# Optimization experiments

Measured on AMD Instinct MI355X. Metric: run time of the kernel, lower is better.

Reference implementation:

```python
import jax, jax.numpy as jnp
import numpy as np

EPS = 1e-7  # K.epsilon()
ROUTINGS = 3


def squash(v, axis=-1):
    s2 = jnp.sum(jnp.square(v), axis=axis, keepdims=True)
    scale = s2 / (1.0 + s2) / jnp.sqrt(s2 + EPS)
    return scale * v


def setup_inputs() -> dict:
    key = jax.random.key(0)
    k1, k2 = jax.random.split(key)
    B, I, D, O, K = 64, 2048, 8, 32, 16
    x = jax.random.normal(k1, (B, I, D), dtype=jnp.float32)
    W = jax.random.normal(k2, (I, O, D, K), dtype=jnp.float32) * 0.05
    return {"x": x, "W": W}


def reference(x, W):
    # u_hat[b,o,i,k] = sum_d x[b,i,d] * W[i,o,d,k]
    u_hat = jnp.einsum('bid,iodk->boik', x, W)  # [B, O, I, K]
    B, O, I, _ = u_hat.shape
    b = jnp.zeros((B, O, I), dtype=u_hat.dtype)
    v = None
    for i in range(ROUTINGS):
        c = jax.nn.softmax(b, axis=1)                      # over output capsules
        s = jnp.einsum('boi,boik->bok', c, u_hat)          # weighted sum
        v = squash(s)                                      # [B, O, K]
        if i < ROUTINGS - 1:
            agreement = jnp.einsum('boik,bok->boi', u_hat, v)
            b = b + agreement
    return v
```

## Files before the change

### kernel.cpp

```cpp
#include <hip/hip_runtime.h>


__device__ __forceinline__ float4 f4add(float4 a, float4 b) {
    return make_float4(a.x + b.x, a.y + b.y, a.z + b.z, a.w + b.w);
}

template<int PASS0>
__global__ __launch_bounds__(512, 4)
void pass_kernel(const float* __restrict__ x,
                 const float* __restrict__ W,
                 const float* __restrict__ vin,
                 float* __restrict__ part)
{
    __shared__ __align__(16) float x_lds[32 * 64];
    __shared__ __align__(16) float red[8 * 2 * 512];
    __shared__ __align__(16) float vg[2 * 512];

    const int t  = threadIdx.x;
    const int w  = t >> 6;
    const int l  = t & 63;
    const int o  = l & 31;
    const int kk = l >> 5;
    const int bx = blockIdx.x;
    const int ch = bx & 255;
    const int h  = bx >> 8;
    const int i  = ch * 8 + w;

    float Wr[8][8];
    {
        const float* wp = W + (size_t)(i * 32 + o) * 128 + kk * 8;
        #pragma unroll
        for (int d = 0; d < 8; ++d) {
            float4 a = *(const float4*)(wp + d * 16);
            float4 b = *(const float4*)(wp + d * 16 + 4);
            Wr[d][0] = a.x; Wr[d][1] = a.y; Wr[d][2] = a.z; Wr[d][3] = a.w;
            Wr[d][4] = b.x; Wr[d][5] = b.y; Wr[d][6] = b.z; Wr[d][7] = b.w;
        }
        #pragma unroll
        for (int d = 0; d < 8; ++d)
            #pragma unroll
            for (int j = 0; j < 8; ++j)
                asm volatile("" : "+v"(Wr[d][j]));
    }
    {
        const int f  = t * 4;
        const int bl = f >> 6, r = f & 63;
        *(float4*)&x_lds[f] =
            *(const float4*)(x + (size_t)(h * 32 + bl) * 16384 + ch * 64 + r);
    }

    for (int g = 0; g < 16; ++g) {
        if (!PASS0) {
            if (t < 256) {
                const int bq = t >> 7, idx = t & 127;
                const int b  = h * 32 + g * 2 + bq;
                *(float4*)&vg[bq * 512 + idx * 4] =
                    *(const float4*)(vin + (size_t)b * 512 + idx * 4);
            }
        }
        __syncthreads();

        #pragma unroll
        for (int bq = 0; bq < 2; ++bq) {
            const int bl = g * 2 + bq;
            float4 xa = *(const float4*)&x_lds[bl * 64 + w * 8];
            float4 xb = *(const float4*)&x_lds[bl * 64 + w * 8 + 4];
            float xr[8] = {xa.x, xa.y, xa.z, xa.w, xb.x, xb.y, xb.z, xb.w};
            float uh[8];
            #pragma unroll
            for (int j = 0; j < 8; ++j) uh[j] = 0.f;
            #pragma unroll
            for (int d = 0; d < 8; ++d) {
                #pragma unroll
                for (int j = 0; j < 8; ++j)
                    uh[j] = fmaf(xr[d], Wr[d][j], uh[j]);
            }
            float c;
            if (PASS0) {
                c = 0.03125f;
            } else {
                float logit = 0.f;
                #pragma unroll
                for (int j = 0; j < 8; ++j)
                    logit = fmaf(uh[j], vg[bq * 512 + (kk * 8 + j) * 32 + o], logit);
                logit += __shfl_xor(logit, 32, 64);
                float ex = __expf(logit);
                float sm = ex;
                #pragma unroll
                for (int off = 16; off >= 1; off >>= 1)
                    sm += __shfl_xor(sm, off, 64);
                c = __fdividef(ex, sm);
            }
            #pragma unroll
            for (int j = 0; j < 8; ++j)
                red[(w * 2 + bq) * 512 + (kk * 8 + j) * 32 + o] = c * uh[j];
        }
        __syncthreads();

        if (t < 256) {
            const int bq = t >> 7, e4 = (t & 127) * 4;
            float4 s = make_float4(0.f, 0.f, 0.f, 0.f);
            #pragma unroll
            for (int slot = 0; slot < 8; ++slot)
                s = f4add(s, *(const float4*)&red[(slot * 2 + bq) * 512 + e4]);
            const int b = h * 32 + g * 2 + bq;
            *(float4*)(part + ((size_t)b * 256 + ch) * 512 + e4) = s;
        }
    }
}

template<int PHASE>
__global__ __launch_bounds__(1024)
void reduce_kernel(const float* __restrict__ part,
                   float* __restrict__ vsum,
                   float* __restrict__ out)
{
    __shared__ float sred[512];
    __shared__ float wpart[8][32];
    const int b = blockIdx.x;
    const int t = threadIdx.x;
    const int e = t & 511;
    const int half = t >> 9;

    const float* p0 = part + ((size_t)b * 256 + half * 128) * 512 + e;
    float acc = 0.f;
    #pragma unroll 8
    for (int cc = 0; cc < 128; ++cc)
        acc += p0[(size_t)cc * 512];

    if (half) sred[e] = acc;
    __syncthreads();

    float s = 0.f;
    if (!half) {
        s = acc + sred[e];
        float sq = s * s;
        sq += __shfl_xor(sq, 32, 64);
        if ((t & 63) < 32) wpart[t >> 6][t & 31] = sq;
    }
    __syncthreads();

    if (!half) {
        float n2 = 0.f;
        #pragma unroll
        for (int ww = 0; ww < 8; ++ww) n2 += wpart[ww][t & 31];
        float v = (n2 / (1.f + n2) * rsqrtf(n2 + 1e-7f)) * s;
        if (PHASE == 2)
            out[(size_t)b * 512 + (t & 31) * 16 + (t >> 5)] = v;
        else if (PHASE == 1)
            vsum[(size_t)b * 512 + t] += v;
        else
            vsum[(size_t)b * 512 + t] = v;
    }
}

extern "C" void kernel_launch(void* const* d_in, const int* in_sizes, int n_in,
                              void* d_out, int out_size, void* d_ws, size_t ws_size,
                              hipStream_t stream)
{
    const float* x = (const float*)d_in[0];
    const float* W = (const float*)d_in[1];
    float* out = (float*)d_out;
    char* ws = (char*)d_ws;

    const size_t partB = (size_t)64 * 256 * 512 * 4;
    const size_t vsumB = (size_t)64 * 512 * 4;
    if (ws_size < partB + vsumB) return;

    float* part = (float*)ws;
    float* vsum = (float*)(ws + partB);

    pass_kernel<1><<<512, 512, 0, stream>>>(x, W, vsum, part);
    reduce_kernel<0><<<64, 1024, 0, stream>>>(part, vsum, out);
    pass_kernel<0><<<512, 512, 0, stream>>>(x, W, vsum, part);
    reduce_kernel<1><<<64, 1024, 0, stream>>>(part, vsum, out);
    pass_kernel<0><<<512, 512, 0, stream>>>(x, W, vsum, part);
    reduce_kernel<2><<<64, 1024, 0, stream>>>(part, vsum, out);
}
```

Measured before the change: 207.0 us.

## Store routing partials in bf16, resplit pass blocks, parallelize reduce with atomics

The pass kernel now assigns 4 input capsules per block, split over two k-halves, and loops over all 64 batches. Each wave holds half of its W slice in registers, and the logit is combined across waves through shared memory. Per-chunk partial sums are written as bf16 instead of fp32, which halves the partial buffer traffic. The reduce kernel becomes 4 blocks per batch that merge with float atomics, and the last-arriving block does the squash. This needs an extra memset and extra barriers, and bf16 partials reduce accuracy.

```diff
diff --git a/kernel.cpp b/kernel.cpp
--- a/kernel.cpp
+++ b/kernel.cpp
@@ -1,4 +1,5 @@
 #include <hip/hip_runtime.h>
+#include <hip/hip_bf16.h>
 
 
 __device__ __forceinline__ float4 f4add(float4 a, float4 b) {
@@ -10,80 +11,83 @@
 void pass_kernel(const float* __restrict__ x,
                  const float* __restrict__ W,
                  const float* __restrict__ vin,
-                 float* __restrict__ part)
+                 unsigned short* __restrict__ part)
 {
-    __shared__ __align__(16) float x_lds[32 * 64];
-    __shared__ __align__(16) float red[8 * 2 * 512];
+    __shared__ __align__(16) float x_lds[2048];
+    __shared__ __align__(16) float red[8 * 512];
     __shared__ __align__(16) float vg[2 * 512];
+    __shared__ float lred[512];
 
     const int t  = threadIdx.x;
-    const int w  = t >> 6;
-    const int l  = t & 63;
-    const int o  = l & 31;
-    const int kk = l >> 5;
-    const int bx = blockIdx.x;
-    const int ch = bx & 255;
-    const int h  = bx >> 8;
-    const int i  = ch * 8 + w;
+    const int w  = t >> 6, l = t & 63;
+    const int iq = w >> 1, q = w & 1;
+    const int o  = l & 31, kk = l >> 5;
+    const int kg = q * 2 + kk;
+    const int ch = blockIdx.x;
+    const int i  = ch * 4 + iq;
 
-    float Wr[8][8];
+    float Wr[8][4];
     {
-        const float* wp = W + (size_t)(i * 32 + o) * 128 + kk * 8;
+        const float* wp = W + (size_t)(i * 32 + o) * 128 + kg * 4;
         #pragma unroll
         for (int d = 0; d < 8; ++d) {
             float4 a = *(const float4*)(wp + d * 16);
-            float4 b = *(const float4*)(wp + d * 16 + 4);
             Wr[d][0] = a.x; Wr[d][1] = a.y; Wr[d][2] = a.z; Wr[d][3] = a.w;
-            Wr[d][4] = b.x; Wr[d][5] = b.y; Wr[d][6] = b.z; Wr[d][7] = b.w;
         }
         #pragma unroll
         for (int d = 0; d < 8; ++d)
             #pragma unroll
-            for (int j = 0; j < 8; ++j)
+            for (int j = 0; j < 4; ++j)
                 asm volatile("" : "+v"(Wr[d][j]));
     }
     {
-        const int f  = t * 4;
-        const int bl = f >> 6, r = f & 63;
-        *(float4*)&x_lds[f] =
-            *(const float4*)(x + (size_t)(h * 32 + bl) * 16384 + ch * 64 + r);
+        const int f = t * 4, b = f >> 5, r = f & 31;
+        *(float4*)&x_lds[f] = *(const float4*)(x + (size_t)b * 16384 + ch * 32 + r);
     }
 
-    for (int g = 0; g < 16; ++g) {
+    for (int g = 0; g < 32; ++g) {
         if (!PASS0) {
             if (t < 256) {
                 const int bq = t >> 7, idx = t & 127;
-                const int b  = h * 32 + g * 2 + bq;
                 *(float4*)&vg[bq * 512 + idx * 4] =
-                    *(const float4*)(vin + (size_t)b * 512 + idx * 4);
+                    *(const float4*)(vin + (size_t)(g * 2 + bq) * 512 + idx * 4);
             }
         }
         __syncthreads();
 
+        float uh[2][4]; float lp[2];
         #pragma unroll
         for (int bq = 0; bq < 2; ++bq) {
-            const int bl = g * 2 + bq;
-            float4 xa = *(const float4*)&x_lds[bl * 64 + w * 8];
-            float4 xb = *(const float4*)&x_lds[bl * 64 + w * 8 + 4];
+            const int b = g * 2 + bq;
+            float4 xa = *(const float4*)&x_lds[b * 32 + iq * 8];
+            float4 xb = *(const float4*)&x_lds[b * 32 + iq * 8 + 4];
             float xr[8] = {xa.x, xa.y, xa.z, xa.w, xb.x, xb.y, xb.z, xb.w};
-            float uh[8];
             #pragma unroll
-            for (int j = 0; j < 8; ++j) uh[j] = 0.f;
+            for (int j = 0; j < 4; ++j) uh[bq][j] = 0.f;
             #pragma unroll
-            for (int d = 0; d < 8; ++d) {
+            for (int d = 0; d < 8; ++d)
                 #pragma unroll
-                for (int j = 0; j < 8; ++j)
-                    uh[j] = fmaf(xr[d], Wr[d][j], uh[j]);
+                for (int j = 0; j < 4; ++j)
+                    uh[bq][j] = fmaf(xr[d], Wr[d][j], uh[bq][j]);
+            if (!PASS0) {
+                float s = 0.f;
+                #pragma unroll
+                for (int j = 0; j < 4; ++j)
+                    s = fmaf(uh[bq][j], vg[bq * 512 + (kg * 4 + j) * 32 + o], s);
+                s += __shfl_xor(s, 32, 64);
+                lp[bq] = s;
+                if (kk == 0) lred[((q * 4 + iq) * 2 + bq) * 32 + o] = s;
             }
+        }
+        if (!PASS0) __syncthreads();
+
+        #pragma unroll
+        for (int bq = 0; bq < 2; ++bq) {
             float c;
             if (PASS0) {
                 c = 0.03125f;
             } else {
-                float logit = 0.f;
-                #pragma unroll
-                for (int j = 0; j < 8; ++j)
-                    logit = fmaf(uh[j], vg[bq * 512 + (kk * 8 + j) * 32 + o], logit);
-                logit += __shfl_xor(logit, 32, 64);
+                float logit = lp[bq] + lred[(((q ^ 1) * 4 + iq) * 2 + bq) * 32 + o];
                 float ex = __expf(logit);
                 float sm = ex;
                 #pragma unroll
@@ -92,8 +96,8 @@
                 c = __fdividef(ex, sm);
             }
             #pragma unroll
-            for (int j = 0; j < 8; ++j)
-                red[(w * 2 + bq) * 512 + (kk * 8 + j) * 32 + o] = c * uh[j];
+            for (int j = 0; j < 4; ++j)
+                red[(iq * 2 + bq) * 512 + (kg * 4 + j) * 32 + o] = c * uh[bq][j];
         }
         __syncthreads();
 
@@ -101,50 +105,57 @@
             const int bq = t >> 7, e4 = (t & 127) * 4;
             float4 s = make_float4(0.f, 0.f, 0.f, 0.f);
             #pragma unroll
-            for (int slot = 0; slot < 8; ++slot)
-                s = f4add(s, *(const float4*)&red[(slot * 2 + bq) * 512 + e4]);
-            const int b = h * 32 + g * 2 + bq;
-            *(float4*)(part + ((size_t)b * 256 + ch) * 512 + e4) = s;
+            for (int q2 = 0; q2 < 4; ++q2)
+                s = f4add(s, *(const float4*)&red[(q2 * 2 + bq) * 512 + e4]);
+            __hip_bfloat16 h0 = __float2bfloat16(s.x), h1 = __float2bfloat16(s.y);
+            __hip_bfloat16 h2 = __float2bfloat16(s.z), h3 = __float2bfloat16(s.w);
+            ushort4 u;
+            u.x = *(unsigned short*)&h0; u.y = *(unsigned short*)&h1;
+            u.z = *(unsigned short*)&h2; u.w = *(unsigned short*)&h3;
+            const int b = g * 2 + bq;
+            *(ushort4*)(part + ((size_t)b * 512 + ch) * 512 + e4) = u;
         }
     }
 }
 
 template<int PHASE>
-__global__ __launch_bounds__(1024)
-void reduce_kernel(const float* __restrict__ part,
-                   float* __restrict__ vsum,
-                   float* __restrict__ out)
+__global__ __launch_bounds__(512)
+void reduce_kernel(const unsigned short* __restrict__ part,
+                   float* __restrict__ s2, int* __restrict__ cnt,
+                   float* __restrict__ vsum, float* __restrict__ out)
 {
-    __shared__ float sred[512];
     __shared__ float wpart[8][32];
-    const int b = blockIdx.x;
+    __shared__ int amLast;
+    const int b = blockIdx.x >> 2, qc = blockIdx.x & 3;
     const int t = threadIdx.x;
-    const int e = t & 511;
-    const int half = t >> 9;
+    const int hh = t >> 8, ee = (t & 255) * 2;
 
-    const float* p0 = part + ((size_t)b * 256 + half * 128) * 512 + e;
-    float acc = 0.f;
-    #pragma unroll 8
-    for (int cc = 0; cc < 128; ++cc)
-        acc += p0[(size_t)cc * 512];
-
-    if (half) sred[e] = acc;
+    const unsigned short* base = part + ((size_t)b * 512 + qc * 128) * 512;
+    float a0 = 0.f, a1 = 0.f;
+    #pragma unroll 4
+    for (int it = 0; it < 64; ++it) {
+        const int row = it * 2 + hh;
+        ushort2 u = *(const ushort2*)(base + (size_t)row * 512 + ee);
+        a0 += __uint_as_float((unsigned)u.x << 16);
+        a1 += __uint_as_float((unsigned)u.y << 16);
+    }
+    atomicAdd(&s2[(size_t)b * 512 + ee],     a0);
+    atomicAdd(&s2[(size_t)b * 512 + ee + 1], a1);
+    __threadfence();
+    __syncthreads();
+    if (t == 0) amLast = (atomicAdd(&cnt[b], 1) == 3);
     __syncthreads();
 
-    float s = 0.f;
-    if (!half) {
-        s = acc + sred[e];
+    if (amLast) {
+        float s = atomicAdd(&s2[(size_t)b * 512 + t], 0.f);
         float sq = s * s;
         sq += __shfl_xor(sq, 32, 64);
         if ((t & 63) < 32) wpart[t >> 6][t & 31] = sq;
-    }
-    __syncthreads();
-
-    if (!half) {
+        __syncthreads();
         float n2 = 0.f;
         #pragma unroll
         for (int ww = 0; ww < 8; ++ww) n2 += wpart[ww][t & 31];
-        float v = (n2 / (1.f + n2) * rsqrtf(n2 + 1e-7f)) * s;
+        float v = n2 / (1.f + n2) * rsqrtf(n2 + 1e-7f) * s;
         if (PHASE == 2)
             out[(size_t)b * 512 + (t & 31) * 16 + (t >> 5)] = v;
         else if (PHASE == 1)
@@ -163,17 +174,23 @@
     float* out = (float*)d_out;
     char* ws = (char*)d_ws;
 
-    const size_t partB = (size_t)64 * 256 * 512 * 4;
+    const size_t partB = (size_t)64 * 512 * 512 * 2;
+    const size_t s2B   = (size_t)3 * 64 * 512 * 4;
+    const size_t cntB  = 1024;
     const size_t vsumB = (size_t)64 * 512 * 4;
-    if (ws_size < partB + vsumB) return;
+    if (ws_size < partB + s2B + cntB + vsumB) return;
 
-    float* part = (float*)ws;
-    float* vsum = (float*)(ws + partB);
+    unsigned short* part = (unsigned short*)ws;
+    float* s2   = (float*)(ws + partB);
+    int*   cnt  = (int*)(ws + partB + s2B);
+    float* vsum = (float*)(ws + partB + s2B + cntB);
+
+    hipMemsetAsync(s2, 0, s2B + cntB, stream);
 
     pass_kernel<1><<<512, 512, 0, stream>>>(x, W, vsum, part);
-    reduce_kernel<0><<<64, 1024, 0, stream>>>(part, vsum, out);
+    reduce_kernel<0><<<256, 512, 0, stream>>>(part, s2,            cnt,       vsum, out);
     pass_kernel<0><<<512, 512, 0, stream>>>(x, W, vsum, part);
-    reduce_kernel<1><<<64, 1024, 0, stream>>>(part, vsum, out);
+    reduce_kernel<1><<<256, 512, 0, stream>>>(part, s2 + 64 * 512, cnt + 64,  vsum, out);
     pass_kernel<0><<<512, 512, 0, stream>>>(x, W, vsum, part);
-    reduce_kernel<2><<<64, 1024, 0, stream>>>(part, vsum, out);
+    reduce_kernel<2><<<256, 512, 0, stream>>>(part, s2 + 2 * 64 * 512, cnt + 128, vsum, out);
 }
```

Result: slower. 343.3 us (+65.9%).

## Split capsule reduction into two-stage kernels and relax pass-kernel occupancy hint

Applied to the files above, without the earlier changes.

The single 64-block reduce kernel, which read the 32 MB partial buffer with scalar loads, is replaced by two kernels. The first uses 256 blocks with float4 loads to reduce chunks into a small intermediate buffer. The second sums the four partials and applies squash. This spreads the memory-bound reduction over more CUs at the cost of an extra launch and workspace per routing iteration. The pass kernel's occupancy hint changes from min 4 blocks to waves_per_eu(2,2), giving the compiler more registers to work with.

```diff
diff --git a/kernel.cpp b/kernel.cpp
--- a/kernel.cpp
+++ b/kernel.cpp
@@ -6,7 +6,8 @@
 }
 
 template<int PASS0>
-__global__ __launch_bounds__(512, 4)
+__global__ __launch_bounds__(512)
+__attribute__((amdgpu_waves_per_eu(2, 2)))
 void pass_kernel(const float* __restrict__ x,
                  const float* __restrict__ W,
                  const float* __restrict__ vin,
@@ -109,49 +110,44 @@
     }
 }
 
+__global__ __launch_bounds__(128)
+void reduce1(const float* __restrict__ part, float* __restrict__ part2)
+{
+    const int b = blockIdx.x >> 2, qc = blockIdx.x & 3;
+    const int t = threadIdx.x;
+    const float* p0 = part + ((size_t)b * 256 + qc * 64) * 512 + t * 4;
+    float4 acc = make_float4(0.f, 0.f, 0.f, 0.f);
+    #pragma unroll 4
+    for (int r = 0; r < 64; ++r)
+        acc = f4add(acc, *(const float4*)(p0 + (size_t)r * 512));
+    *(float4*)(part2 + ((size_t)b * 4 + qc) * 512 + t * 4) = acc;
+}
+
 template<int PHASE>
-__global__ __launch_bounds__(1024)
-void reduce_kernel(const float* __restrict__ part,
-                   float* __restrict__ vsum,
-                   float* __restrict__ out)
+__global__ __launch_bounds__(512)
+void reduce2(const float* __restrict__ part2, float* __restrict__ vsum,
+             float* __restrict__ out)
 {
-    __shared__ float sred[512];
     __shared__ float wpart[8][32];
-    const int b = blockIdx.x;
-    const int t = threadIdx.x;
-    const int e = t & 511;
-    const int half = t >> 9;
-
-    const float* p0 = part + ((size_t)b * 256 + half * 128) * 512 + e;
-    float acc = 0.f;
-    #pragma unroll 8
-    for (int cc = 0; cc < 128; ++cc)
-        acc += p0[(size_t)cc * 512];
-
-    if (half) sred[e] = acc;
+    const int b = blockIdx.x, t = threadIdx.x;
+    float s = 0.f;
+    #pragma unroll
+    for (int qc = 0; qc < 4; ++qc)
+        s += part2[((size_t)b * 4 + qc) * 512 + t];
+    float sq = s * s;
+    sq += __shfl_xor(sq, 32, 64);
+    if ((t & 63) < 32) wpart[t >> 6][t & 31] = sq;
     __syncthreads();
-
-    float s = 0.f;
-    if (!half) {
-        s = acc + sred[e];
-        float sq = s * s;
-        sq += __shfl_xor(sq, 32, 64);
-        if ((t & 63) < 32) wpart[t >> 6][t & 31] = sq;
-    }
-    __syncthreads();
-
-    if (!half) {
-        float n2 = 0.f;
-        #pragma unroll
-        for (int ww = 0; ww < 8; ++ww) n2 += wpart[ww][t & 31];
-        float v = (n2 / (1.f + n2) * rsqrtf(n2 + 1e-7f)) * s;
-        if (PHASE == 2)
-            out[(size_t)b * 512 + (t & 31) * 16 + (t >> 5)] = v;
-        else if (PHASE == 1)
-            vsum[(size_t)b * 512 + t] += v;
-        else
-            vsum[(size_t)b * 512 + t] = v;
-    }
+    float n2 = 0.f;
+    #pragma unroll
+    for (int ww = 0; ww < 8; ++ww) n2 += wpart[ww][t & 31];
+    float v = n2 / (1.f + n2) * rsqrtf(n2 + 1e-7f) * s;
+    if (PHASE == 2)
+        out[(size_t)b * 512 + (t & 31) * 16 + (t >> 5)] = v;
+    else if (PHASE == 1)
+        vsum[(size_t)b * 512 + t] += v;
+    else
+        vsum[(size_t)b * 512 + t] = v;
 }
 
 extern "C" void kernel_launch(void* const* d_in, const int* in_sizes, int n_in,
@@ -163,17 +159,22 @@
     float* out = (float*)d_out;
     char* ws = (char*)d_ws;
 
-    const size_t partB = (size_t)64 * 256 * 512 * 4;
-    const size_t vsumB = (size_t)64 * 512 * 4;
-    if (ws_size < partB + vsumB) return;
+    const size_t partB  = (size_t)64 * 256 * 512 * 4;
+    const size_t part2B = (size_t)64 * 4 * 512 * 4;
+    const size_t vsumB  = (size_t)64 * 512 * 4;
+    if (ws_size < partB + part2B + vsumB) return;
 
-    float* part = (float*)ws;
-    float* vsum = (float*)(ws + partB);
+    float* part  = (float*)ws;
+    float* part2 = (float*)(ws + partB);
+    float* vsum  = (float*)(ws + partB + part2B);
 
     pass_kernel<1><<<512, 512, 0, stream>>>(x, W, vsum, part);
-    reduce_kernel<0><<<64, 1024, 0, stream>>>(part, vsum, out);
+    reduce1<<<256, 128, 0, stream>>>(part, part2);
+    reduce2<0><<<64, 512, 0, stream>>>(part2, vsum, out);
     pass_kernel<0><<<512, 512, 0, stream>>>(x, W, vsum, part);
-    reduce_kernel<1><<<64, 1024, 0, stream>>>(part, vsum, out);
+    reduce1<<<256, 128, 0, stream>>>(part, part2);
+    reduce2<1><<<64, 512, 0, stream>>>(part2, vsum, out);
     pass_kernel<0><<<512, 512, 0, stream>>>(x, W, vsum, part);
-    reduce_kernel<2><<<64, 1024, 0, stream>>>(part, vsum, out);
+    reduce1<<<256, 128, 0, stream>>>(part, part2);
+    reduce2<2><<<64, 512, 0, stream>>>(part2, vsum, out);
 }
```

New measurement: 256.8 us. 1.24x slower.
